# Kernel tuning notes

Hardware: AMD Instinct MI355X
Metric: run time of the kernel (lower is better)

Reference implementation:

```python
import jax, jax.numpy as jnp
import numpy as np

K1, K2, ALPHA = 0.01, 0.03, 0.84
SIGMA_LEVELS = (1, 2, 4, 7)

def _box_conv(x, k):
    # x: [B,1,H,W]; uniform k x k mean filter, padding k//2 (matches F.conv2d)
    p = k // 2
    w = jnp.ones((1, 1, k, k), x.dtype) / (k * k)
    return jax.lax.conv_general_dilated(
        x, w, window_strides=(1, 1), padding=((p, p), (p, p)),
        dimension_numbers=('NCHW', 'OIHW', 'NCHW'))

def _ssim_mean(X, Y, C1, C2, k):
    ux = _box_conv(X, k)
    uy = _box_conv(Y, k)
    uxx = _box_conv(X * X, k)
    uyy = _box_conv(Y * Y, k)
    uxy = _box_conv(X * Y, k)
    vx = uxx - ux * ux
    vy = uyy - uy * uy
    vxy = uxy - ux * uy
    A1 = 2 * ux * uy + C1
    A2 = 2 * vxy + C2
    B1 = ux * ux + uy * uy + C1
    B2 = vx + vy + C2
    S = (A1 * A2) / (B1 * B2)
    return jnp.mean(S)

def setup_inputs() -> dict:
    key = jax.random.key(0)
    k1, k2 = jax.random.split(key)
    B, H, W = 128, 384, 384
    X = jax.random.uniform(k1, (B, H, W), dtype=jnp.float32)
    Y = jax.random.uniform(k2, (B, H, W), dtype=jnp.float32)
    data_range = jnp.ones((B,), dtype=jnp.float32)
    return {"X": X, "Y": Y, "data_range": data_range}

def reference(X, Y, data_range):
    X4 = X[:, None, :, :]   # [B,1,H,W]
    Y4 = Y[:, None, :, :]
    dr = data_range[:, None, None, None]  # [B,1,1,1]
    C1 = (K1 * dr) ** 2
    C2 = (K2 * dr) ** 2
    # msssim = product of scalar SSIM means over sigma levels (ones_like * scalars).mean()
    msssim = jnp.float32(1.0)
    for k in SIGMA_LEVELS:
        msssim = msssim * _ssim_mean(X4, Y4, C1, C2, k)
    msssim_loss = 1.0 - msssim
    kM = SIGMA_LEVELS[-1]
    fX = _box_conv(X4, kM)
    fY = _box_conv(Y4, kM)
    l1 = jnp.mean(jnp.abs(fX - fY))
    return ALPHA * msssim_loss + (1.0 - ALPHA) * l1
```

## Files before the change

kernel.cpp:

```cpp
#include <hip/hip_runtime.h>


#define W 384
#define H 384
#define NB 128
#define BAND 48
#define NTILES 7
#define NBLK (NTILES * 2 * NB)

__device__ __forceinline__ float bp(int addr, float v) {
    return __int_as_float(__builtin_amdgcn_ds_bpermute(addr, __float_as_int(v)));
}

__device__ __forceinline__ float ssim_pm(const float* V, float k2, float c1k42, float c2k42) {
    const float p2 = V[0] * V[0];
    const float m2 = V[1] * V[1];
    const float d  = p2 - m2;
    const float s  = p2 + m2;
    const float dq = V[2] - V[3];
    const float sq = V[2] + V[3];
    const float A1 = d + c1k42;
    const float B1 = s + c1k42;
    const float A2 = fmaf(k2, dq, -d) + c2k42;
    const float B2 = fmaf(k2, sq, -s) + c2k42;
    return (A1 * A2) * __builtin_amdgcn_rcpf(B1 * B2);
}

__global__ __launch_bounds__(256) void msssim_main(
    const float* __restrict__ X, const float* __restrict__ Y,
    const float* __restrict__ dr, float* __restrict__ part)
{
    const int lane = threadIdx.x & 63;
    const int wv   = threadIdx.x >> 6;
    const int tile = blockIdx.x;
    const int band = blockIdx.y * 4 + wv;
    const int b    = blockIdx.z;

    const int cbase = -3 + 56 * tile;
    const int c     = cbase + lane;
    const int R0    = BAND * band;

    const int g1hi  = R0 + 48;
    const int g24hi = (band == 7) ? 385 : R0 + 48;

    const float drb = dr[b];
    const float C1 = (0.01f * drb) * (0.01f * drb);
    const float C2 = (0.03f * drb) * (0.03f * drb);
    const float tC1 = 2.f * C1;
    const float C1_2 = C1 * 32.f,    C2_2 = C2 * 32.f;
    const float C1_4 = C1 * 512.f,   C2_4 = C2 * 512.f;
    const float C1_7 = C1 * 4802.f,  C2_7 = C2 * 4802.f;

    const float m1 = (lane >= 3 && lane <= 58 && c     <= 383) ? 1.f : 0.f;
    const float m2 = (lane >= 2 && lane <= 57 && c + 1 <= 384) ? 1.f : 0.f;
    const float m4 = (lane >= 1 && lane <= 56 && c + 2 <= 384) ? 1.f : 0.f;
    const float m7 = (             lane <= 55 && c + 3 <= 383) ? 1.f : 0.f;

    const float mcol = (c >= 0 && c < W) ? 1.f : 0.f;
    const int   cc   = c < 0 ? 0 : (c > W - 1 ? W - 1 : c);

    const int a1 = ((lane + 1) & 63) << 2;
    const int a2 = ((lane + 2) & 63) << 2;
    const int a4 = ((lane + 4) & 63) << 2;
    const int a6 = ((lane + 6) & 63) << 2;

    const float* __restrict__ Xb = X + (size_t)b * (H * W);
    const float* __restrict__ Yb = Y + (size_t)b * (H * W);

    float r2[4], r4[3][4], r7[6][4], v4s[4], v7s[4];
#pragma unroll
    for (int q = 0; q < 4; ++q) {
        r2[q] = 0.f;
        r4[0][q] = r4[1][q] = r4[2][q] = 0.f;
#pragma unroll
        for (int a = 0; a < 6; ++a) r7[a][q] = 0.f;
        v4s[q] = 0.f; v7s[q] = 0.f;
    }

    float ss1 = 0.f, ss2 = 0.f, ss4 = 0.f, ss7 = 0.f, l1 = 0.f;

    const int u0 = R0 - 3;

    float px[6], py[6];
    auto loadv = [&](int u, float& x, float& y) {
        if (u >= 0 && u < H) {
            x = Xb[(size_t)u * W + cc];
            y = Yb[(size_t)u * W + cc];
        } else { x = 0.f; y = 0.f; }
    };

    float SA[14], SB[14];
    auto stage = [&](float xr, float yr, float* S) {
        const float pv  = (xr + yr) * mcol;
        const float mv  = (xr - yr) * mcol;
        const float ppv = pv * pv;
        const float mmv = mv * mv;
        S[12] = ppv; S[13] = mmv;
        const float qv[4] = { pv, mv, ppv, mmv };
#pragma unroll
        for (int q = 0; q < 4; ++q) {
            const float v   = qv[q];
            const float sh1 = bp(a1, v);
            const float t   = v + sh1;
            const float sh2 = bp(a2, t);
            const float sh4 = bp(a4, t);
            const float sh6 = bp(a6, v);
            const float w4  = t + sh2;
            S[q]     = t;
            S[4 + q] = w4;
            S[8 + q] = w4 + (sh4 + sh6);
        }
    };

    loadv(u0,     px[0], py[0]);
    loadv(u0 + 1, px[1], py[1]);
    loadv(u0 + 2, px[2], py[2]);
    stage(px[0], py[0], SA);

    for (int s = 0; s < 54; s += 6) {
#pragma unroll
        for (int ph = 0; ph < 6; ++ph) {
            const int u = u0 + s + ph;

            loadv(u + 3, px[(ph + 3) % 6], py[(ph + 3) % 6]);

            const bool evenT = ((ph & 1) == 0);
            float* Sn       = evenT ? SB : SA;
            const float* Sv = evenT ? SA : SB;
            stage(px[(ph + 1) % 6], py[(ph + 1) % 6], Sn);

            float V2[4], V4[4], V7[4];
#pragma unroll
            for (int q = 0; q < 4; ++q) {
                const float w2v = Sv[q], w4v = Sv[4 + q], w7v = Sv[8 + q];
                V2[q] = w2v + r2[q];  r2[q] = w2v;
                const float a4v = w4v + v4s[q];
                V4[q] = a4v;  v4s[q] = a4v - r4[2][q];
                r4[2][q] = r4[1][q]; r4[1][q] = r4[0][q]; r4[0][q] = w4v;
                const float a7v = w7v + v7s[q];
                V7[q] = a7v;  v7s[q] = a7v - r7[5][q];
                r7[5][q] = r7[4][q]; r7[4][q] = r7[3][q]; r7[3][q] = r7[2][q];
                r7[2][q] = r7[1][q]; r7[1][q] = r7[0][q]; r7[0][q] = w7v;
            }

            if (u >= R0 && u < g1hi) {
                const float num = (Sv[12] - Sv[13]) + tC1;
                const float den = (Sv[12] + Sv[13]) + tC1;
                ss1 = fmaf(num * __builtin_amdgcn_rcpf(den), m1, ss1);
            }
            if (u >= R0 && u < g24hi) {
                ss2 = fmaf(ssim_pm(V2, 4.f, C1_2, C2_2), m2, ss2);
            }
            {
                const int i = u - 1;
                if (i >= R0 && i < g24hi) {
                    ss4 = fmaf(ssim_pm(V4, 16.f, C1_4, C2_4), m4, ss4);
                }
            }
            {
                const int i = u - 3;
                if (i >= R0 && i < g1hi) {
                    ss7 = fmaf(ssim_pm(V7, 49.f, C1_7, C2_7), m7, ss7);
                    l1  = fmaf(fabsf(V7[1]), m7, l1);
                }
            }
        }
    }

#pragma unroll
    for (int d = 32; d > 0; d >>= 1) {
        ss1 += __shfl_down(ss1, d, 64);
        ss2 += __shfl_down(ss2, d, 64);
        ss4 += __shfl_down(ss4, d, 64);
        ss7 += __shfl_down(ss7, d, 64);
        l1  += __shfl_down(l1,  d, 64);
    }
    __shared__ float sred[4][5];
    if (lane == 0) {
        sred[wv][0] = ss1; sred[wv][1] = ss2; sred[wv][2] = ss4;
        sred[wv][3] = ss7; sred[wv][4] = l1;
    }
    __syncthreads();
    if (threadIdx.x == 0) {
        const int bid = ((int)blockIdx.z * 2 + (int)blockIdx.y) * NTILES + (int)blockIdx.x;
#pragma unroll
        for (int q = 0; q < 5; ++q)
            part[bid * 5 + q] = sred[0][q] + sred[1][q] + sred[2][q] + sred[3][q];
    }
}

__global__ __launch_bounds__(256) void reduce_final(
    const float* __restrict__ part, float* __restrict__ out)
{
    const int lane = threadIdx.x & 63;
    const int wv   = threadIdx.x >> 6;
    double d[5] = {0, 0, 0, 0, 0};
    for (int i = threadIdx.x; i < NBLK; i += 256) {
#pragma unroll
        for (int q = 0; q < 5; ++q) d[q] += (double)part[i * 5 + q];
    }
#pragma unroll
    for (int s = 32; s > 0; s >>= 1) {
#pragma unroll
        for (int q = 0; q < 5; ++q) d[q] += __shfl_down(d[q], s, 64);
    }
    __shared__ double sd[4][5];
    if (lane == 0) {
#pragma unroll
        for (int q = 0; q < 5; ++q) sd[wv][q] = d[q];
    }
    __syncthreads();
    if (threadIdx.x == 0) {
        double a[5];
#pragma unroll
        for (int q = 0; q < 5; ++q)
            a[q] = sd[0][q] + sd[1][q] + sd[2][q] + sd[3][q];
        const double n384 = (double)NB * 384.0 * 384.0;
        const double n385 = (double)NB * 385.0 * 385.0;
        const double m  = (a[0] / n384) * (a[1] / n385) * (a[2] / n385) * (a[3] / n384);
        const double l1 = a[4] / 49.0 / n384;
        out[0] = (float)(0.84 * (1.0 - m) + 0.16 * l1);
    }
}

extern "C" void kernel_launch(void* const* d_in, const int* in_sizes, int n_in,
                              void* d_out, int out_size, void* d_ws, size_t ws_size,
                              hipStream_t stream) {
    const float* X  = (const float*)d_in[0];
    const float* Y  = (const float*)d_in[1];
    const float* dr = (const float*)d_in[2];
    float* out  = (float*)d_out;
    float* part = (float*)d_ws;

    dim3 grid(NTILES, 2, NB);
    msssim_main<<<grid, 256, 0, stream>>>(X, Y, dr, part);
    reduce_final<<<1, 256, 0, stream>>>(part, out);
}
```

Baseline: 223.1 us.

## Process two columns per lane with float2 loads and packed math

Each lane now owns two adjacent columns, loaded as a float2, so a wavefront covers 112 output columns instead of 56 and the grid drops from 7 to 4 column strips. The horizontal window sums are built from only three cross-lane permutes of p and m per row; the squared terms are formed by squaring the shuffled values, not permuted separately. The SSIM math runs on float2 vectors so the compiler can emit packed FP32 instructions. The change cuts halo redundancy and the number of ds_bpermute operations per output, at the cost of roughly double the register state per lane, which may lower occupancy.

```diff
diff --git a/kernel.cpp b/kernel.cpp
--- a/kernel.cpp
+++ b/kernel.cpp
@@ -5,25 +5,35 @@
 #define H 384
 #define NB 128
 #define BAND 48
-#define NTILES 7
-#define NBLK (NTILES * 2 * NB)
+#define NSTRIPS 4
+#define NBLK (NSTRIPS * 2 * NB)
+
+typedef __attribute__((ext_vector_type(2))) float f2;
 
 __device__ __forceinline__ float bp(int addr, float v) {
     return __int_as_float(__builtin_amdgcn_ds_bpermute(addr, __float_as_int(v)));
 }
 
-__device__ __forceinline__ float ssim_pm(const float* V, float k2, float c1k42, float c2k42) {
-    const float p2 = V[0] * V[0];
-    const float m2 = V[1] * V[1];
-    const float d  = p2 - m2;
-    const float s  = p2 + m2;
-    const float dq = V[2] - V[3];
-    const float sq = V[2] + V[3];
-    const float A1 = d + c1k42;
-    const float B1 = s + c1k42;
-    const float A2 = fmaf(k2, dq, -d) + c2k42;
-    const float B2 = fmaf(k2, sq, -s) + c2k42;
-    return (A1 * A2) * __builtin_amdgcn_rcpf(B1 * B2);
+__device__ __forceinline__ f2 f2s(float v) { f2 r; r.x = v; r.y = v; return r; }
+
+__device__ __forceinline__ f2 ssim_pm2(f2 Vp, f2 Vm, f2 Vpp, f2 Vmm,
+                                       float k2, float c1k42, float c2k42) {
+    const f2 p2 = Vp * Vp;
+    const f2 m2 = Vm * Vm;
+    const f2 d  = p2 - m2;
+    const f2 s  = p2 + m2;
+    const f2 dq = Vpp - Vmm;
+    const f2 sq = Vpp + Vmm;
+    const f2 A1 = d + c1k42;
+    const f2 B1 = s + c1k42;
+    const f2 A2 = __builtin_elementwise_fma(f2s(k2), dq, -d) + c2k42;
+    const f2 B2 = __builtin_elementwise_fma(f2s(k2), sq, -s) + c2k42;
+    const f2 num = A1 * A2;
+    const f2 den = B1 * B2;
+    f2 r;
+    r.x = num.x * __builtin_amdgcn_rcpf(den.x);
+    r.y = num.y * __builtin_amdgcn_rcpf(den.y);
+    return r;
 }
 
 __global__ __launch_bounds__(256) void msssim_main(
@@ -32,13 +42,13 @@
 {
     const int lane = threadIdx.x & 63;
     const int wv   = threadIdx.x >> 6;
-    const int tile = blockIdx.x;
+    const int strip= blockIdx.x;
     const int band = blockIdx.y * 4 + wv;
     const int b    = blockIdx.z;
 
-    const int cbase = -3 + 56 * tile;
-    const int c     = cbase + lane;
-    const int R0    = BAND * band;
+    const int i0 = 112 * strip - 4 + 2 * lane;
+    const int i1 = i0 + 1;
+    const int R0 = BAND * band;
 
     const int g1hi  = R0 + 48;
     const int g24hi = (band == 7) ? 385 : R0 + 48;
@@ -51,122 +61,171 @@
     const float C1_4 = C1 * 512.f,   C2_4 = C2 * 512.f;
     const float C1_7 = C1 * 4802.f,  C2_7 = C2 * 4802.f;
 
-    const float m1 = (lane >= 3 && lane <= 58 && c     <= 383) ? 1.f : 0.f;
-    const float m2 = (lane >= 2 && lane <= 57 && c + 1 <= 384) ? 1.f : 0.f;
-    const float m4 = (lane >= 1 && lane <= 56 && c + 2 <= 384) ? 1.f : 0.f;
-    const float m7 = (             lane <= 55 && c + 3 <= 383) ? 1.f : 0.f;
-
-    const float mcol = (c >= 0 && c < W) ? 1.f : 0.f;
-    const int   cc   = c < 0 ? 0 : (c > W - 1 ? W - 1 : c);
-
-    const int a1 = ((lane + 1) & 63) << 2;
-    const int a2 = ((lane + 2) & 63) << 2;
-    const int a4 = ((lane + 4) & 63) << 2;
-    const int a6 = ((lane + 6) & 63) << 2;
-
-    const float* __restrict__ Xb = X + (size_t)b * (H * W);
-    const float* __restrict__ Yb = Y + (size_t)b * (H * W);
-
-    float r2[4], r4[3][4], r7[6][4], v4s[4], v7s[4];
+    const int lo   = 112 * strip;
+    const int hi17 = (lo + 112 < 384) ? lo + 112 : 384;
+    const int hi24 = (lo + 112 < 385) ? lo + 112 : 385;
+    auto own = [&](int j, int hi) -> float {
+        return (j >= lo && j < hi) ? 1.f : 0.f;
+    };
+    const f2 mk1 = { own(i0,     hi17), own(i1,     hi17) };
+    const f2 mk2 = { own(i0 + 1, hi24), own(i1 + 1, hi24) };
+    const f2 mk4 = { own(i0 + 2, hi24), own(i1 + 2, hi24) };
+    const f2 mk7 = { own(i0 + 3, hi17), own(i1 + 3, hi17) };
+
+    f2 mc;
+    mc.x = (i0 >= 0 && i0 < W) ? 1.f : 0.f;
+    mc.y = (i1 >= 0 && i1 < W) ? 1.f : 0.f;
+    const int cE = i0 < 0 ? 0 : (i0 > W - 2 ? W - 2 : i0);
+
+    const int ba1 = ((lane + 1) & 63) << 2;
+    const int ba2 = ((lane + 2) & 63) << 2;
+    const int ba3 = ((lane + 3) & 63) << 2;
+
+    const float* __restrict__ Xr = X + (size_t)b * (H * W) + cE;
+    const float* __restrict__ Yr = Y + (size_t)b * (H * W) + cE;
+
+    f2 r2[4], r4[3][4], r7[6][4], v4s[4], v7s[4];
 #pragma unroll
     for (int q = 0; q < 4; ++q) {
-        r2[q] = 0.f;
-        r4[0][q] = r4[1][q] = r4[2][q] = 0.f;
-#pragma unroll
-        for (int a = 0; a < 6; ++a) r7[a][q] = 0.f;
-        v4s[q] = 0.f; v7s[q] = 0.f;
-    }
-
-    float ss1 = 0.f, ss2 = 0.f, ss4 = 0.f, ss7 = 0.f, l1 = 0.f;
+        r2[q] = f2s(0.f);
+        r4[0][q] = r4[1][q] = r4[2][q] = f2s(0.f);
+#pragma unroll
+        for (int a = 0; a < 6; ++a) r7[a][q] = f2s(0.f);
+        v4s[q] = f2s(0.f); v7s[q] = f2s(0.f);
+    }
+
+    f2 ss1v = f2s(0.f), ss2v = f2s(0.f), ss4v = f2s(0.f),
+       ss7v = f2s(0.f), l1v  = f2s(0.f);
 
     const int u0 = R0 - 3;
 
-    float px[6], py[6];
-    auto loadv = [&](int u, float& x, float& y) {
+    f2 rx[3], ry[3];
+    auto loadv = [&](int u, int slot) {
         if (u >= 0 && u < H) {
-            x = Xb[(size_t)u * W + cc];
-            y = Yb[(size_t)u * W + cc];
-        } else { x = 0.f; y = 0.f; }
-    };
-
-    float SA[14], SB[14];
-    auto stage = [&](float xr, float yr, float* S) {
-        const float pv  = (xr + yr) * mcol;
-        const float mv  = (xr - yr) * mcol;
-        const float ppv = pv * pv;
-        const float mmv = mv * mv;
-        S[12] = ppv; S[13] = mmv;
-        const float qv[4] = { pv, mv, ppv, mmv };
-#pragma unroll
-        for (int q = 0; q < 4; ++q) {
-            const float v   = qv[q];
-            const float sh1 = bp(a1, v);
-            const float t   = v + sh1;
-            const float sh2 = bp(a2, t);
-            const float sh4 = bp(a4, t);
-            const float sh6 = bp(a6, v);
-            const float w4  = t + sh2;
-            S[q]     = t;
-            S[4 + q] = w4;
-            S[8 + q] = w4 + (sh4 + sh6);
-        }
-    };
-
-    loadv(u0,     px[0], py[0]);
-    loadv(u0 + 1, px[1], py[1]);
-    loadv(u0 + 2, px[2], py[2]);
-    stage(px[0], py[0], SA);
+            rx[slot] = *(const f2*)(Xr + (size_t)u * W);
+            ry[slot] = *(const f2*)(Yr + (size_t)u * W);
+        } else { rx[slot] = f2s(0.f); ry[slot] = f2s(0.f); }
+    };
+
+    f2 sp[3], sm[3];
+    float sr[3][12];
+    auto stageRow = [&](int ps, int bs) {
+        const f2 p = (rx[ps] + ry[ps]) * mc;
+        const f2 m = (rx[ps] - ry[ps]) * mc;
+        sp[bs] = p; sm[bs] = m;
+        sr[bs][0]  = bp(ba1, p.x);  sr[bs][1]  = bp(ba1, p.y);
+        sr[bs][2]  = bp(ba2, p.x);  sr[bs][3]  = bp(ba2, p.y);
+        sr[bs][4]  = bp(ba3, p.x);  sr[bs][5]  = bp(ba3, p.y);
+        sr[bs][6]  = bp(ba1, m.x);  sr[bs][7]  = bp(ba1, m.y);
+        sr[bs][8]  = bp(ba2, m.x);  sr[bs][9]  = bp(ba2, m.y);
+        sr[bs][10] = bp(ba3, m.x);  sr[bs][11] = bp(ba3, m.y);
+    };
+
+    auto hwin = [&](f2 v0, float e2, float e3, float e4, float e5,
+                    float e6, float e7, f2& w2, f2& w4, f2& w7) {
+        const float w2a = v0.x + v0.y;
+        const float w2b = v0.y + e2;
+        const float t1  = e2 + e3;
+        const float w4a = w2a + t1;
+        const float t1b = e3 + e4;
+        const float w4b = w2b + t1b;
+        const float t2  = e4 + e5;
+        const float w7a = (w4a + t2) + e6;
+        const float t3  = e5 + e6;
+        const float w7b = (w4b + t3) + e7;
+        w2.x = w2a; w2.y = w2b;
+        w4.x = w4a; w4.y = w4b;
+        w7.x = w7a; w7.y = w7b;
+    };
+
+    loadv(u0,     0);
+    loadv(u0 + 1, 1);
+    loadv(u0 + 2, 2);
+    stageRow(0, 0);
+    stageRow(1, 1);
+    loadv(u0 + 3, 0);
 
     for (int s = 0; s < 54; s += 6) {
 #pragma unroll
         for (int ph = 0; ph < 6; ++ph) {
             const int u = u0 + s + ph;
 
-            loadv(u + 3, px[(ph + 3) % 6], py[(ph + 3) % 6]);
-
-            const bool evenT = ((ph & 1) == 0);
-            float* Sn       = evenT ? SB : SA;
-            const float* Sv = evenT ? SA : SB;
-            stage(px[(ph + 1) % 6], py[(ph + 1) % 6], Sn);
-
-            float V2[4], V4[4], V7[4];
+            loadv(u + 4, (ph + 1) % 3);
+
+            const int cb = ph % 3;
+            const f2 p0 = sp[cb], m0 = sm[cb];
+            const float pa1 = sr[cb][0],  pb1 = sr[cb][1];
+            const float pa2 = sr[cb][2],  pb2 = sr[cb][3];
+            const float pa3 = sr[cb][4],  pb3 = sr[cb][5];
+            const float ma1 = sr[cb][6],  mb1 = sr[cb][7];
+            const float ma2 = sr[cb][8],  mb2 = sr[cb][9];
+            const float ma3 = sr[cb][10], mb3 = sr[cb][11];
+
+            const f2 pp0 = p0 * p0;
+            const f2 mm0 = m0 * m0;
+
+            f2 W2[4], W4[4], W7[4];
+            hwin(p0,  pa1, pb1, pa2, pb2, pa3, pb3, W2[0], W4[0], W7[0]);
+            hwin(m0,  ma1, mb1, ma2, mb2, ma3, mb3, W2[1], W4[1], W7[1]);
+            hwin(pp0, pa1*pa1, pb1*pb1, pa2*pa2, pb2*pb2, pa3*pa3, pb3*pb3,
+                 W2[2], W4[2], W7[2]);
+            hwin(mm0, ma1*ma1, mb1*mb1, ma2*ma2, mb2*mb2, ma3*ma3, mb3*mb3,
+                 W2[3], W4[3], W7[3]);
+
+            f2 V2[4], V4[4], V7[4];
 #pragma unroll
             for (int q = 0; q < 4; ++q) {
-                const float w2v = Sv[q], w4v = Sv[4 + q], w7v = Sv[8 + q];
-                V2[q] = w2v + r2[q];  r2[q] = w2v;
-                const float a4v = w4v + v4s[q];
+                V2[q] = W2[q] + r2[q];  r2[q] = W2[q];
+                const f2 a4v = W4[q] + v4s[q];
                 V4[q] = a4v;  v4s[q] = a4v - r4[2][q];
-                r4[2][q] = r4[1][q]; r4[1][q] = r4[0][q]; r4[0][q] = w4v;
-                const float a7v = w7v + v7s[q];
+                r4[2][q] = r4[1][q]; r4[1][q] = r4[0][q]; r4[0][q] = W4[q];
+                const f2 a7v = W7[q] + v7s[q];
                 V7[q] = a7v;  v7s[q] = a7v - r7[5][q];
                 r7[5][q] = r7[4][q]; r7[4][q] = r7[3][q]; r7[3][q] = r7[2][q];
-                r7[2][q] = r7[1][q]; r7[1][q] = r7[0][q]; r7[0][q] = w7v;
+                r7[2][q] = r7[1][q]; r7[1][q] = r7[0][q]; r7[0][q] = W7[q];
             }
 
             if (u >= R0 && u < g1hi) {
-                const float num = (Sv[12] - Sv[13]) + tC1;
-                const float den = (Sv[12] + Sv[13]) + tC1;
-                ss1 = fmaf(num * __builtin_amdgcn_rcpf(den), m1, ss1);
+                const f2 num = (pp0 - mm0) + tC1;
+                const f2 den = (pp0 + mm0) + tC1;
+                f2 s1;
+                s1.x = num.x * __builtin_amdgcn_rcpf(den.x);
+                s1.y = num.y * __builtin_amdgcn_rcpf(den.y);
+                ss1v = __builtin_elementwise_fma(s1, mk1, ss1v);
             }
             if (u >= R0 && u < g24hi) {
-                ss2 = fmaf(ssim_pm(V2, 4.f, C1_2, C2_2), m2, ss2);
+                ss2v = __builtin_elementwise_fma(
+                    ssim_pm2(V2[0], V2[1], V2[2], V2[3], 4.f, C1_2, C2_2),
+                    mk2, ss2v);
             }
             {
                 const int i = u - 1;
                 if (i >= R0 && i < g24hi) {
-                    ss4 = fmaf(ssim_pm(V4, 16.f, C1_4, C2_4), m4, ss4);
+                    ss4v = __builtin_elementwise_fma(
+                        ssim_pm2(V4[0], V4[1], V4[2], V4[3], 16.f, C1_4, C2_4),
+                        mk4, ss4v);
                 }
             }
             {
                 const int i = u - 3;
                 if (i >= R0 && i < g1hi) {
-                    ss7 = fmaf(ssim_pm(V7, 49.f, C1_7, C2_7), m7, ss7);
-                    l1  = fmaf(fabsf(V7[1]), m7, l1);
+                    ss7v = __builtin_elementwise_fma(
+                        ssim_pm2(V7[0], V7[1], V7[2], V7[3], 49.f, C1_7, C2_7),
+                        mk7, ss7v);
+                    f2 av; av.x = fabsf(V7[1].x); av.y = fabsf(V7[1].y);
+                    l1v = __builtin_elementwise_fma(av, mk7, l1v);
                 }
             }
+
+            stageRow((ph + 2) % 3, (ph + 2) % 3);
         }
     }
 
+    float ss1 = ss1v.x + ss1v.y;
+    float ss2 = ss2v.x + ss2v.y;
+    float ss4 = ss4v.x + ss4v.y;
+    float ss7 = ss7v.x + ss7v.y;
+    float l1  = l1v.x  + l1v.y;
 #pragma unroll
     for (int d = 32; d > 0; d >>= 1) {
         ss1 += __shfl_down(ss1, d, 64);
@@ -182,7 +241,7 @@
     }
     __syncthreads();
     if (threadIdx.x == 0) {
-        const int bid = ((int)blockIdx.z * 2 + (int)blockIdx.y) * NTILES + (int)blockIdx.x;
+        const int bid = ((int)blockIdx.z * 2 + (int)blockIdx.y) * NSTRIPS + (int)blockIdx.x;
 #pragma unroll
         for (int q = 0; q < 5; ++q)
             part[bid * 5 + q] = sred[0][q] + sred[1][q] + sred[2][q] + sred[3][q];
@@ -232,7 +291,7 @@
     float* out  = (float*)d_out;
     float* part = (float*)d_ws;
 
-    dim3 grid(NTILES, 2, NB);
+    dim3 grid(NSTRIPS, 2, NB);
     msssim_main<<<grid, 256, 0, stream>>>(X, Y, dr, part);
     reduce_final<<<1, 256, 0, stream>>>(part, out);
 }
```

New measurement: 201.1 us. -9.8%, faster.
